# Performance work log

Hardware: AMD Instinct MI355X
Metric: run time of the kernel (lower is better)

The kernel has to match this reference:

```python
import jax, jax.numpy as jnp
import numpy as np

B, S, H = 16, 8192, 256


def setup_inputs() -> dict:
    key = jax.random.key(0)
    k1, k2, k3, k4, k5, k6 = jax.random.split(key, 6)
    # He/Glorot-ish scaling for the linear layer is irrelevant for correctness; use small randn.
    return {
        "query": jax.random.normal(k1, (B, 1, H), dtype=jnp.float32),
        "key": jax.random.normal(k2, (B, S, H), dtype=jnp.float32),
        "value": jax.random.normal(k3, (B, S, H), dtype=jnp.float32),
        "W_attn": jax.random.normal(k4, (H, 2 * H), dtype=jnp.float32) * 0.05,  # nn.Linear(2H, H).weight
        "b_attn": jax.random.normal(k5, (H,), dtype=jnp.float32) * 0.05,
        "v": jax.random.uniform(k6, (H,), dtype=jnp.float32),  # torch.rand init
    }


def reference(query, key, value, W_attn, b_attn, v):
    # Faithful to: tanh(Linear(cat([query.repeat(S), key], -1))) @ v -> softmax -> weighted sum.
    # Split the Linear weight so we never materialize the repeated/concatenated [B,S,2H] tensor:
    # cat([q,k]) @ W.T == q @ Wq.T + k @ Wk.T, with Wq = W[:, :H], Wk = W[:, H:].
    Wq = W_attn[:, :H]  # [H, H]
    Wk = W_attn[:, H:]  # [H, H]
    hidden = jnp.tanh(
        jnp.einsum("bqh,oh->bqo", query, Wq)        # [B,1,H], broadcasts over S
        + jnp.einsum("bsh,oh->bso", key, Wk)        # [B,S,H]
        + b_attn
    )  # [B,S,H]
    scores = jnp.einsum("bsh,h->bs", hidden, v)      # [B,S]
    attn_weights = jax.nn.softmax(scores, axis=-1)   # softmax over sequence
    context = jnp.einsum("bs,bsh->bh", attn_weights, value)[:, None, :]  # [B,1,H]
    return context, attn_weights
```

## Files before the change

### kernel.cpp

```cpp
#include <hip/hip_runtime.h>

#define B_SZ 16
#define S_SZ 8192
#define H_SZ 256

typedef _Float16 half8 __attribute__((ext_vector_type(8)));
typedef float f32x4 __attribute__((ext_vector_type(4)));

__device__ __forceinline__ float tanh_fast(float x) {
  float e = __expf(2.0f * x);
  return 1.0f - 2.0f / (e + 1.0f);
}

__global__ __launch_bounds__(256) void prep_kernel(
    const float* __restrict__ query, const float* __restrict__ W_attn,
    const float* __restrict__ b_attn, float* __restrict__ qb) {
  const int b = blockIdx.x;
  const int jo = blockIdx.y;
  const int wid = threadIdx.x >> 6;
  const int lane = threadIdx.x & 63;
  const float4 q4 = *(const float4*)(query + b * H_SZ + lane * 4);
#pragma unroll 4
  for (int i = 0; i < 16; i++) {
    const int o = jo * 64 + wid * 16 + i;
    const float4 w = *(const float4*)(W_attn + (size_t)o * 512 + lane * 4);
    float p = q4.x * w.x + q4.y * w.y + q4.z * w.z + q4.w * w.w;
#pragma unroll
    for (int off = 32; off >= 1; off >>= 1) p += __shfl_xor(p, off, 64);
    if (lane == 0) qb[b * H_SZ + o] = p + b_attn[o];
  }
}

__global__ __launch_bounds__(1024, 4) void fused_kernel(
    const float* __restrict__ key, const float* __restrict__ value,
    const float* __restrict__ W_attn, const float* __restrict__ qb,
    const float* __restrict__ vvec, float* __restrict__ scores,
    float* __restrict__ ctxp, float* __restrict__ mblk,
    float* __restrict__ zblk) {
  __shared__ __align__(16) _Float16 kbuf[2][32 * 256];
  __shared__ float psum[8][32];
  __shared__ float4 comb[16][64];

  const int tid = threadIdx.x;
  const int wid = tid >> 6;
  const int lane = tid & 63;
  const int n = lane & 15;
  const int quad = lane >> 4;
  const int rowBase = blockIdx.x * 256;
  const int b = blockIdx.x >> 5;

  half8 afrag[8];
  {
    const float* wrow = W_attn + (size_t)(wid * 16 + n) * 512 + 256 + quad * 8;
#pragma unroll
    for (int ks = 0; ks < 8; ks++) {
      float4 f0 = *(const float4*)(wrow + ks * 32);
      float4 f1 = *(const float4*)(wrow + ks * 32 + 4);
      half8 a;
      a[0] = (_Float16)f0.x; a[1] = (_Float16)f0.y;
      a[2] = (_Float16)f0.z; a[3] = (_Float16)f0.w;
      a[4] = (_Float16)f1.x; a[5] = (_Float16)f1.y;
      a[6] = (_Float16)f1.z; a[7] = (_Float16)f1.w;
      afrag[ks] = a;
    }
  }
  float qbv[4], vvv[4];
#pragma unroll
  for (int rg = 0; rg < 4; rg++) {
    qbv[rg] = qb[b * H_SZ + wid * 16 + quad * 4 + rg];
    vvv[rg] = vvec[wid * 16 + quad * 4 + rg];
  }

  if (tid < 256) ((float*)psum)[tid] = 0.f;

  const int srow = tid >> 5;
  const int sseg = tid & 31;
  const size_t sbase = (size_t)(rowBase + srow) * H_SZ + sseg * 8;
  const int sdst = srow * 256 + ((sseg ^ srow) << 3);

  const float* vbase = value + (size_t)(rowBase + 2 * wid) * H_SZ + lane * 4;

  {
    float4 f0 = *(const float4*)(key + sbase);
    float4 f1 = *(const float4*)(key + sbase + 4);
    half8 h;
    h[0] = (_Float16)f0.x; h[1] = (_Float16)f0.y;
    h[2] = (_Float16)f0.z; h[3] = (_Float16)f0.w;
    h[4] = (_Float16)f1.x; h[5] = (_Float16)f1.y;
    h[6] = (_Float16)f1.z; h[7] = (_Float16)f1.w;
    *(half8*)&kbuf[0][sdst] = h;
  }
  __syncthreads();

  float4 acc4 = {0.f, 0.f, 0.f, 0.f};
  float m_run = -1e30f;
  float z_run = 0.f;

  for (int c = 0; c < 8; c++) {
    const float4 va0 = *(const float4*)(vbase + (size_t)c * 32 * H_SZ);
    const float4 va1 = *(const float4*)(vbase + (size_t)c * 32 * H_SZ + H_SZ);
    float4 g0, g1;
    if (c < 7) {
      const size_t nb = sbase + (size_t)(c + 1) * 32 * H_SZ;
      g0 = *(const float4*)(key + nb);
      g1 = *(const float4*)(key + nb + 4);
    }
    const _Float16* kb = kbuf[c & 1];
#pragma unroll
    for (int rt = 0; rt < 2; rt++) {
      const int lrow = rt * 16 + n;
      f32x4 acc = {0.f, 0.f, 0.f, 0.f};
#pragma unroll
      for (int ks = 0; ks < 8; ks++) {
        half8 bfrag =
            *(const half8*)&kb[lrow * 256 + (((ks * 4 + quad) ^ lrow) << 3)];
        acc = __builtin_amdgcn_mfma_f32_16x16x32_f16(afrag[ks], bfrag, acc,
                                                     0, 0, 0);
      }
      float p = 0.f;
#pragma unroll
      for (int rg = 0; rg < 4; rg++)
        p = fmaf(vvv[rg], tanh_fast(qbv[rg] + acc[rg]), p);
      p += __shfl_xor(p, 16, 64);
      p += __shfl_xor(p, 32, 64);
      if (quad == 0) atomicAdd(&psum[c][lrow], p);
    }
    if (c < 7) {
      half8 h;
      h[0] = (_Float16)g0.x; h[1] = (_Float16)g0.y;
      h[2] = (_Float16)g0.z; h[3] = (_Float16)g0.w;
      h[4] = (_Float16)g1.x; h[5] = (_Float16)g1.y;
      h[6] = (_Float16)g1.z; h[7] = (_Float16)g1.w;
      *(half8*)&kbuf[(c + 1) & 1][sdst] = h;
    }
    __syncthreads();

    const float sv = psum[c][lane & 31];
    float cm = sv;
#pragma unroll
    for (int off = 16; off >= 1; off >>= 1)
      cm = fmaxf(cm, __shfl_xor(cm, off, 64));
    const float m_new = fmaxf(m_run, cm);
    const float scl = __expf(m_run - m_new);
    m_run = m_new;
    const float wl = __expf(sv - m_new);
    if (wid == 0) {
      if (lane < 32) scores[rowBase + c * 32 + lane] = sv;
      float zc = wl;
#pragma unroll
      for (int off = 16; off >= 1; off >>= 1) zc += __shfl_xor(zc, off, 64);
      z_run = fmaf(z_run, scl, zc);
    }
    const float w0 = __shfl(wl, 2 * wid + 0, 64);
    const float w1 = __shfl(wl, 2 * wid + 1, 64);
    acc4.x = fmaf(w1, va1.x, fmaf(w0, va0.x, acc4.x * scl));
    acc4.y = fmaf(w1, va1.y, fmaf(w0, va0.y, acc4.y * scl));
    acc4.z = fmaf(w1, va1.z, fmaf(w0, va0.z, acc4.z * scl));
    acc4.w = fmaf(w1, va1.w, fmaf(w0, va0.w, acc4.w * scl));
  }

  comb[wid][lane] = acc4;
  __syncthreads();
  if (tid < 64) {
    float4 t4 = comb[0][tid];
#pragma unroll
    for (int j = 1; j < 16; j++) {
      const float4 u = comb[j][tid];
      t4.x += u.x; t4.y += u.y; t4.z += u.z; t4.w += u.w;
    }
    *(float4*)(ctxp + (size_t)blockIdx.x * 256 + tid * 4) = t4;
  }
  if (tid == 0) {
    mblk[blockIdx.x] = m_run;
    zblk[blockIdx.x] = z_run;
  }
}

__global__ __launch_bounds__(1024) void combine_kernel(
    const float* __restrict__ ctxp, const float* __restrict__ mblk,
    const float* __restrict__ zblk, float* __restrict__ attn,
    float* __restrict__ ctx) {
  const int b = blockIdx.x;
  const int t = threadIdx.x;
  __shared__ float ms[32], zs[32];
  if (t < 32) {
    ms[t] = mblk[b * 32 + t];
    zs[t] = zblk[b * 32 + t];
  }
  __syncthreads();
  float m = -1e30f;
#pragma unroll
  for (int j = 0; j < 32; j++) m = fmaxf(m, ms[j]);
  float Z = 0.f;
  float e[32];
#pragma unroll
  for (int j = 0; j < 32; j++) {
    e[j] = __expf(ms[j] - m);
    Z = fmaf(zs[j], e[j], Z);
  }
  const float invZ = 1.0f / Z;
  if (t < 256) {
    float acc = 0.f;
#pragma unroll
    for (int j = 0; j < 32; j++)
      acc = fmaf(ctxp[(size_t)(b * 32 + j) * 256 + t], e[j], acc);
    ctx[b * H_SZ + t] = acc * invZ;
  }
  float* arow = attn + (size_t)b * S_SZ;
#pragma unroll
  for (int k = 0; k < 8; k++) {
    const int idx = k * 1024 + t;
    arow[idx] = __expf(arow[idx] - m) * invZ;
  }
}

extern "C" void kernel_launch(void* const* d_in, const int* in_sizes, int n_in,
                              void* d_out, int out_size, void* d_ws,
                              size_t ws_size, hipStream_t stream) {
  const float* query = (const float*)d_in[0];
  const float* key = (const float*)d_in[1];
  const float* value = (const float*)d_in[2];
  const float* W_attn = (const float*)d_in[3];
  const float* b_attn = (const float*)d_in[4];
  const float* vvec = (const float*)d_in[5];

  float* out = (float*)d_out;
  float* ctx = out;
  float* attn = out + 4096;
  float* ctxp = (float*)d_ws;
  float* mblk = ctxp + 512 * 256;
  float* zblk = mblk + 512;

  prep_kernel<<<dim3(B_SZ, 4), 256, 0, stream>>>(query, W_attn, b_attn, ctx);
  fused_kernel<<<512, 1024, 0, stream>>>(key, value, W_attn, ctx, vvec, attn,
                                         ctxp, mblk, zblk);
  combine_kernel<<<B_SZ, 1024, 0, stream>>>(ctxp, mblk, zblk, attn, ctx);
}
```

Before: 311.7 us.

## Halve fused block to 512 threads with two output tiles per wave; split normalize kernel

The fused kernel now runs 8 waves per block instead of 16. Each wave holds two 16-row W fragments and issues two MFMAs per key fragment load, so each staged key fragment is reused twice. Each thread stages two key rows, and the q/v vectors move to shared memory to save registers. The final attn normalization moves into a separate wide-grid kernel so it no longer runs on only 16 blocks, at the cost of one extra launch and less parallelism per block in the fused kernel.

```diff
diff --git a/kernel.cpp b/kernel.cpp
--- a/kernel.cpp
+++ b/kernel.cpp
@@ -31,7 +31,7 @@
   }
 }
 
-__global__ __launch_bounds__(1024, 4) void fused_kernel(
+__global__ __launch_bounds__(512, 4) void fused_kernel(
     const float* __restrict__ key, const float* __restrict__ value,
     const float* __restrict__ W_attn, const float* __restrict__ qb,
     const float* __restrict__ vvec, float* __restrict__ scores,
@@ -39,19 +39,22 @@
     float* __restrict__ zblk) {
   __shared__ __align__(16) _Float16 kbuf[2][32 * 256];
   __shared__ float psum[8][32];
-  __shared__ float4 comb[16][64];
+  __shared__ float2 qv[256];
+  __shared__ float4 comb[8][64];
 
   const int tid = threadIdx.x;
-  const int wid = tid >> 6;
+  const int w = tid >> 6;
   const int lane = tid & 63;
   const int n = lane & 15;
   const int quad = lane >> 4;
   const int rowBase = blockIdx.x * 256;
   const int b = blockIdx.x >> 5;
 
-  half8 afrag[8];
-  {
-    const float* wrow = W_attn + (size_t)(wid * 16 + n) * 512 + 256 + quad * 8;
+  half8 afrag[2][8];
+#pragma unroll
+  for (int ot = 0; ot < 2; ot++) {
+    const float* wrow =
+        W_attn + (size_t)(w * 32 + ot * 16 + n) * 512 + 256 + quad * 8;
 #pragma unroll
     for (int ks = 0; ks < 8; ks++) {
       float4 f0 = *(const float4*)(wrow + ks * 32);
@@ -61,35 +64,38 @@
       a[2] = (_Float16)f0.z; a[3] = (_Float16)f0.w;
       a[4] = (_Float16)f1.x; a[5] = (_Float16)f1.y;
       a[6] = (_Float16)f1.z; a[7] = (_Float16)f1.w;
-      afrag[ks] = a;
-    }
-  }
-  float qbv[4], vvv[4];
-#pragma unroll
-  for (int rg = 0; rg < 4; rg++) {
-    qbv[rg] = qb[b * H_SZ + wid * 16 + quad * 4 + rg];
-    vvv[rg] = vvec[wid * 16 + quad * 4 + rg];
-  }
-
-  if (tid < 256) ((float*)psum)[tid] = 0.f;
-
-  const int srow = tid >> 5;
+      afrag[ot][ks] = a;
+    }
+  }
+  if (tid < 256) {
+    qv[tid] = make_float2(qb[b * H_SZ + tid], vvec[tid]);
+    ((float*)psum)[tid] = 0.f;
+  }
+
   const int sseg = tid & 31;
-  const size_t sbase = (size_t)(rowBase + srow) * H_SZ + sseg * 8;
-  const int sdst = srow * 256 + ((sseg ^ srow) << 3);
-
-  const float* vbase = value + (size_t)(rowBase + 2 * wid) * H_SZ + lane * 4;
-
-  {
-    float4 f0 = *(const float4*)(key + sbase);
-    float4 f1 = *(const float4*)(key + sbase + 4);
-    half8 h;
-    h[0] = (_Float16)f0.x; h[1] = (_Float16)f0.y;
-    h[2] = (_Float16)f0.z; h[3] = (_Float16)f0.w;
-    h[4] = (_Float16)f1.x; h[5] = (_Float16)f1.y;
-    h[6] = (_Float16)f1.z; h[7] = (_Float16)f1.w;
-    *(half8*)&kbuf[0][sdst] = h;
-  }
+  const int srow0 = tid >> 5;
+  const int srow1 = srow0 + 16;
+  const size_t sb0 = (size_t)(rowBase + srow0) * H_SZ + sseg * 8;
+  const size_t sb1 = (size_t)(rowBase + srow1) * H_SZ + sseg * 8;
+  const int sd0 = srow0 * 256 + ((sseg ^ srow0) << 3);
+  const int sd1 = srow1 * 256 + ((sseg ^ srow1) << 3);
+
+  const float* vbase = value + (size_t)(rowBase + 4 * w) * H_SZ + lane * 4;
+
+#define STAGE_PASS(buf, sb, sd, coff)                                   \
+  do {                                                                  \
+    float4 f0 = *(const float4*)(key + (sb) + (coff));                  \
+    float4 f1 = *(const float4*)(key + (sb) + (coff) + 4);              \
+    half8 h;                                                            \
+    h[0] = (_Float16)f0.x; h[1] = (_Float16)f0.y;                       \
+    h[2] = (_Float16)f0.z; h[3] = (_Float16)f0.w;                       \
+    h[4] = (_Float16)f1.x; h[5] = (_Float16)f1.y;                       \
+    h[6] = (_Float16)f1.z; h[7] = (_Float16)f1.w;                       \
+    *(half8*)&kbuf[buf][sd] = h;                                        \
+  } while (0)
+
+  STAGE_PASS(0, sb0, sd0, 0);
+  STAGE_PASS(0, sb1, sd1, 0);
   __syncthreads();
 
   float4 acc4 = {0.f, 0.f, 0.f, 0.f};
@@ -97,41 +103,44 @@
   float z_run = 0.f;
 
   for (int c = 0; c < 8; c++) {
-    const float4 va0 = *(const float4*)(vbase + (size_t)c * 32 * H_SZ);
-    const float4 va1 = *(const float4*)(vbase + (size_t)c * 32 * H_SZ + H_SZ);
-    float4 g0, g1;
-    if (c < 7) {
-      const size_t nb = sbase + (size_t)(c + 1) * 32 * H_SZ;
-      g0 = *(const float4*)(key + nb);
-      g1 = *(const float4*)(key + nb + 4);
-    }
+    const size_t coff = (size_t)c * 32 * H_SZ;
+    const float4 va0 = *(const float4*)(vbase + coff);
+    const float4 va1 = *(const float4*)(vbase + coff + H_SZ);
+
     const _Float16* kb = kbuf[c & 1];
 #pragma unroll
     for (int rt = 0; rt < 2; rt++) {
       const int lrow = rt * 16 + n;
-      f32x4 acc = {0.f, 0.f, 0.f, 0.f};
+      f32x4 acc0 = {0.f, 0.f, 0.f, 0.f};
+      f32x4 acc1 = {0.f, 0.f, 0.f, 0.f};
 #pragma unroll
       for (int ks = 0; ks < 8; ks++) {
         half8 bfrag =
             *(const half8*)&kb[lrow * 256 + (((ks * 4 + quad) ^ lrow) << 3)];
-        acc = __builtin_amdgcn_mfma_f32_16x16x32_f16(afrag[ks], bfrag, acc,
-                                                     0, 0, 0);
+        acc0 = __builtin_amdgcn_mfma_f32_16x16x32_f16(afrag[0][ks], bfrag,
+                                                      acc0, 0, 0, 0);
+        acc1 = __builtin_amdgcn_mfma_f32_16x16x32_f16(afrag[1][ks], bfrag,
+                                                      acc1, 0, 0, 0);
       }
       float p = 0.f;
 #pragma unroll
-      for (int rg = 0; rg < 4; rg++)
-        p = fmaf(vvv[rg], tanh_fast(qbv[rg] + acc[rg]), p);
+      for (int rg = 0; rg < 4; rg++) {
+        const int o0 = w * 32 + quad * 4 + rg;
+        const float2 q0 = qv[o0];
+        const float2 q1 = qv[o0 + 16];
+        p = fmaf(q0.y, tanh_fast(q0.x + acc0[rg]), p);
+        p = fmaf(q1.y, tanh_fast(q1.x + acc1[rg]), p);
+      }
       p += __shfl_xor(p, 16, 64);
       p += __shfl_xor(p, 32, 64);
       if (quad == 0) atomicAdd(&psum[c][lrow], p);
     }
+    const float4 vb0 = *(const float4*)(vbase + coff + 2 * H_SZ);
+    const float4 vb1 = *(const float4*)(vbase + coff + 3 * H_SZ);
     if (c < 7) {
-      half8 h;
-      h[0] = (_Float16)g0.x; h[1] = (_Float16)g0.y;
-      h[2] = (_Float16)g0.z; h[3] = (_Float16)g0.w;
-      h[4] = (_Float16)g1.x; h[5] = (_Float16)g1.y;
-      h[6] = (_Float16)g1.z; h[7] = (_Float16)g1.w;
-      *(half8*)&kbuf[(c + 1) & 1][sdst] = h;
+      const size_t noff = coff + 32 * H_SZ;
+      STAGE_PASS((c + 1) & 1, sb0, sd0, noff);
+      STAGE_PASS((c + 1) & 1, sb1, sd1, noff);
     }
     __syncthreads();
 
@@ -144,27 +153,34 @@
     const float scl = __expf(m_run - m_new);
     m_run = m_new;
     const float wl = __expf(sv - m_new);
-    if (wid == 0) {
+    if (w == 0) {
       if (lane < 32) scores[rowBase + c * 32 + lane] = sv;
       float zc = wl;
 #pragma unroll
       for (int off = 16; off >= 1; off >>= 1) zc += __shfl_xor(zc, off, 64);
       z_run = fmaf(z_run, scl, zc);
     }
-    const float w0 = __shfl(wl, 2 * wid + 0, 64);
-    const float w1 = __shfl(wl, 2 * wid + 1, 64);
-    acc4.x = fmaf(w1, va1.x, fmaf(w0, va0.x, acc4.x * scl));
-    acc4.y = fmaf(w1, va1.y, fmaf(w0, va0.y, acc4.y * scl));
-    acc4.z = fmaf(w1, va1.z, fmaf(w0, va0.z, acc4.z * scl));
-    acc4.w = fmaf(w1, va1.w, fmaf(w0, va0.w, acc4.w * scl));
-  }
-
-  comb[wid][lane] = acc4;
+    const float w0 = __shfl(wl, 4 * w + 0, 64);
+    const float w1 = __shfl(wl, 4 * w + 1, 64);
+    const float w2 = __shfl(wl, 4 * w + 2, 64);
+    const float w3 = __shfl(wl, 4 * w + 3, 64);
+    acc4.x = fmaf(w3, vb1.x,
+             fmaf(w2, vb0.x, fmaf(w1, va1.x, fmaf(w0, va0.x, acc4.x * scl))));
+    acc4.y = fmaf(w3, vb1.y,
+             fmaf(w2, vb0.y, fmaf(w1, va1.y, fmaf(w0, va0.y, acc4.y * scl))));
+    acc4.z = fmaf(w3, vb1.z,
+             fmaf(w2, vb0.z, fmaf(w1, va1.z, fmaf(w0, va0.z, acc4.z * scl))));
+    acc4.w = fmaf(w3, vb1.w,
+             fmaf(w2, vb0.w, fmaf(w1, va1.w, fmaf(w0, va0.w, acc4.w * scl))));
+  }
+#undef STAGE_PASS
+
+  comb[w][lane] = acc4;
   __syncthreads();
   if (tid < 64) {
     float4 t4 = comb[0][tid];
 #pragma unroll
-    for (int j = 1; j < 16; j++) {
+    for (int j = 1; j < 8; j++) {
       const float4 u = comb[j][tid];
       t4.x += u.x; t4.y += u.y; t4.z += u.z; t4.w += u.w;
     }
@@ -176,10 +192,10 @@
   }
 }
 
-__global__ __launch_bounds__(1024) void combine_kernel(
+__global__ __launch_bounds__(256) void combine_kernel(
     const float* __restrict__ ctxp, const float* __restrict__ mblk,
-    const float* __restrict__ zblk, float* __restrict__ attn,
-    float* __restrict__ ctx) {
+    const float* __restrict__ zblk, float* __restrict__ ctx,
+    float* __restrict__ mf, float* __restrict__ zf) {
   const int b = blockIdx.x;
   const int t = threadIdx.x;
   __shared__ float ms[32], zs[32];
@@ -198,20 +214,27 @@
     e[j] = __expf(ms[j] - m);
     Z = fmaf(zs[j], e[j], Z);
   }
-  const float invZ = 1.0f / Z;
-  if (t < 256) {
-    float acc = 0.f;
-#pragma unroll
-    for (int j = 0; j < 32; j++)
-      acc = fmaf(ctxp[(size_t)(b * 32 + j) * 256 + t], e[j], acc);
-    ctx[b * H_SZ + t] = acc * invZ;
-  }
+  float acc = 0.f;
+#pragma unroll
+  for (int j = 0; j < 32; j++)
+    acc = fmaf(ctxp[(size_t)(b * 32 + j) * 256 + t], e[j], acc);
+  ctx[b * H_SZ + t] = acc / Z;
+  if (t == 0) {
+    mf[b] = m;
+    zf[b] = Z;
+  }
+}
+
+__global__ __launch_bounds__(512) void normalize_kernel(
+    const float* __restrict__ mf, const float* __restrict__ zf,
+    float* __restrict__ attn) {
+  const int b = blockIdx.x;
+  const int j = blockIdx.y;
+  const float m = mf[b];
+  const float invZ = 1.0f / zf[b];
+  const int idx = j * 512 + threadIdx.x;
   float* arow = attn + (size_t)b * S_SZ;
-#pragma unroll
-  for (int k = 0; k < 8; k++) {
-    const int idx = k * 1024 + t;
-    arow[idx] = __expf(arow[idx] - m) * invZ;
-  }
+  arow[idx] = __expf(arow[idx] - m) * invZ;
 }
 
 extern "C" void kernel_launch(void* const* d_in, const int* in_sizes, int n_in,
@@ -230,9 +253,12 @@
   float* ctxp = (float*)d_ws;
   float* mblk = ctxp + 512 * 256;
   float* zblk = mblk + 512;
+  float* mf = zblk + 512;
+  float* zf = mf + 16;
 
   prep_kernel<<<dim3(B_SZ, 4), 256, 0, stream>>>(query, W_attn, b_attn, ctx);
-  fused_kernel<<<512, 1024, 0, stream>>>(key, value, W_attn, ctx, vvec, attn,
-                                         ctxp, mblk, zblk);
-  combine_kernel<<<B_SZ, 1024, 0, stream>>>(ctxp, mblk, zblk, attn, ctx);
-}
+  fused_kernel<<<512, 512, 0, stream>>>(key, value, W_attn, ctx, vvec, attn,
+                                        ctxp, mblk, zblk);
+  combine_kernel<<<B_SZ, 256, 0, stream>>>(ctxp, mblk, zblk, ctx, mf, zf);
+  normalize_kernel<<<dim3(B_SZ, 16), 512, 0, stream>>>(mf, zf, attn);
+}
```

Result: slower. 361.6 us (+16.0%).
